# Performance work log

Hardware: AMD Instinct MI355X
Metric: run time of the kernel (lower is better)

## Reference

```python
import jax, jax.numpy as jnp
import numpy as np
import math

B, L, D = 8, 1024, 512
H, DK, DV = 8, 64, 64
DFC = 2048
EPS = 1e-5


def layernorm(x, g, b):
    mu = jnp.mean(x, axis=-1, keepdims=True)
    var = jnp.var(x, axis=-1, keepdims=True)
    return (x - mu) * jax.lax.rsqrt(var + EPS) * g + b


def setup_inputs() -> dict:
    key = jax.random.key(0)
    ks = jax.random.split(key, 12)
    s = 0.02
    return {
        "x": jax.random.normal(ks[0], (B, L, D), jnp.float32),
        "Wq": jax.random.normal(ks[1], (H * DK, D), jnp.float32) * s,
        "bq": jnp.zeros((H * DK,), jnp.float32),
        "Wk": jax.random.normal(ks[2], (H * DK, D), jnp.float32) * s,
        "bk": jnp.zeros((H * DK,), jnp.float32),
        "Wv": jax.random.normal(ks[3], (H * DV, D), jnp.float32) * s,
        "bv": jnp.zeros((H * DV,), jnp.float32),
        "Wo": jax.random.normal(ks[4], (D, H * DV), jnp.float32) * s,
        "bo": jnp.zeros((D,), jnp.float32),
        "conv1_w": jax.random.normal(ks[5], (DFC, D), jnp.float32) * s,
        "conv1_b": jnp.zeros((DFC,), jnp.float32),
        "ln1_g": jnp.ones((D,), jnp.float32),
        "ln1_b": jnp.zeros((D,), jnp.float32),
        "conv2_w": jax.random.normal(ks[6], (D, DFC), jnp.float32) * s,
        "conv2_b": jnp.zeros((D,), jnp.float32),
        "ln2_g": jnp.ones((D,), jnp.float32),
        "ln2_b": jnp.zeros((D,), jnp.float32),
    }


def reference(x, Wq, bq, Wk, bk, Wv, bv, Wo, bo, conv1_w, conv1_b,
              ln1_g, ln1_b, conv2_w, conv2_b, ln2_g, ln2_b):
    # Multihead attention (self-attn: x supplies Q,K and V)
    norm_fact = 1.0 / math.sqrt(D)
    Q = (x @ Wq.T + bq).reshape(B, L, H, DK)
    K = (x @ Wk.T + bk).reshape(B, L, H, DK)
    V = (x @ Wv.T + bv).reshape(B, L, H, DV)
    scores = jnp.einsum('blhe,bshe->bhls', Q, K) * norm_fact  # [B,H,L,L]
    scores = jax.nn.softmax(scores, axis=-1)
    attn_out = jnp.einsum('bhls,bshd->blhd', scores, V).reshape(B, L, H * DV)
    x_ = attn_out @ Wo.T + bo
    # residual + LayerNorm (dropout is identity in eval)
    x1 = layernorm(x + x_, ln1_g, ln1_b)
    # pointwise conv FFN (kernel_size=1 == linear over channels)
    y = jax.nn.relu(jnp.einsum('bld,fd->blf', x1, conv1_w) + conv1_b)
    y = jnp.einsum('blf,df->bld', y, conv2_w) + conv2_b
    return layernorm(x1 + y, ln2_g, ln2_b)
```

## Files before the change

### kernel.cpp

```cpp
#include <hip/hip_runtime.h>
#include <hip/hip_bf16.h>
#include <math.h>

#define Bp 8
#define Lp 1024
#define Dp 512
#define Hp 8
#define DFCp 2048
#define ROWS (Bp*Lp)
#define EPSp 1e-5f
#define SCALEp 0.04419417382415922f

typedef __bf16 bf16_t;
typedef __attribute__((ext_vector_type(8))) __bf16 bf16x8;
typedef __attribute__((ext_vector_type(4))) __bf16 bf16x4;
typedef __attribute__((ext_vector_type(4))) float f32x4;

__global__ __launch_bounds__(256) void f2b_all(
    const float* __restrict__ x,  const float* __restrict__ Wq,
    const float* __restrict__ Wk, const float* __restrict__ Wv,
    const float* __restrict__ Wo, const float* __restrict__ c1,
    const float* __restrict__ c2,
    bf16_t* __restrict__ xb, bf16_t* __restrict__ WQKVb,
    bf16_t* __restrict__ Wob, bf16_t* __restrict__ c1b,
    bf16_t* __restrict__ c2b)
{
    int i = blockIdx.x * 256 + threadIdx.x;
    const float* src; bf16_t* dst; int off;
    if      (i < 1048576) { src = x;  dst = xb;              off = i; }
    else if (i < 1114112) { src = Wq; dst = WQKVb;           off = i - 1048576; }
    else if (i < 1179648) { src = Wk; dst = WQKVb + 262144;  off = i - 1114112; }
    else if (i < 1245184) { src = Wv; dst = WQKVb + 524288;  off = i - 1179648; }
    else if (i < 1310720) { src = Wo; dst = Wob;             off = i - 1245184; }
    else if (i < 1572864) { src = c1; dst = c1b;             off = i - 1310720; }
    else                  { src = c2; dst = c2b;             off = i - 1572864; }
    float4 v = ((const float4*)src)[off];
    bf16x4 o;
    o[0] = (bf16_t)v.x; o[1] = (bf16_t)v.y; o[2] = (bf16_t)v.z; o[3] = (bf16_t)v.w;
    ((bf16x4*)dst)[off] = o;
}

__global__ __launch_bounds__(256) void pack_bias(const float* __restrict__ bq,
                                                 const float* __restrict__ bk,
                                                 const float* __restrict__ bv,
                                                 float* __restrict__ out) {
    int i = blockIdx.x * 256 + threadIdx.x;
    float v;
    if (i < 512) v = bq[i];
    else if (i < 1024) v = bk[i - 512];
    else v = bv[i - 1024];
    out[i] = v;
}

__device__ __forceinline__ void gload16(const bf16_t* g, bf16_t* l) {
    __builtin_amdgcn_global_load_lds(
        (const __attribute__((address_space(1))) void*)g,
        (__attribute__((address_space(3))) void*)l,
        16, 0, 0);
}

template<int OUT_BF16, int RELU, int SPLIT_V, int NT, int KSPLIT>
__global__ __launch_bounds__(256) void gemm_mfma(
    const bf16_t* __restrict__ A, const bf16_t* __restrict__ W,
    const float* __restrict__ bias, void* __restrict__ Cv,
    bf16_t* __restrict__ Ct, bf16_t* __restrict__ P0, bf16_t* __restrict__ P1,
    int M, int N, int Kd)
{
    constexpr int NJ = NT / 32;
    __shared__ bf16_t As[128 * 32];
    __shared__ bf16_t Bs[NT * 32];
    const int tid  = threadIdx.x;
    const int wave = tid >> 6;
    const int lane = tid & 63;
    const int row0 = blockIdx.y * 128;
    const int col0 = blockIdx.x * NT;
    const int wm = (wave >> 1) * 64;
    const int wn = (wave & 1) * (NT / 2);

    const int sr = lane >> 2;
    const int sc = (lane & 3) * 8;
    const int half = lane >> 4;
    const int mrow = lane & 15;

    f32x4 acc[4][NJ] = {};

    const bf16_t* Ag = A + (size_t)row0 * Kd;
    const bf16_t* Bg = W + (size_t)col0 * Kd;

    const int Kc = Kd / KSPLIT;
    const int kbeg = (KSPLIT > 1) ? blockIdx.z * Kc : 0;

    for (int k0 = kbeg; k0 < kbeg + Kc; k0 += 32) {
        __syncthreads();
        #pragma unroll
        for (int c = 0; c < 2; ++c) {
            const int chunk = c * 4 + wave;
            const int r = chunk * 16 + sr;
            gload16(Ag + (size_t)r * Kd + k0 + sc, &As[chunk * 512]);
        }
        #pragma unroll
        for (int c = 0; c < NT / 64; ++c) {
            const int chunk = c * 4 + wave;
            const int r = chunk * 16 + sr;
            gload16(Bg + (size_t)r * Kd + k0 + sc, &Bs[chunk * 512]);
        }
        __syncthreads();

        bf16x8 af[4], bfr[NJ];
        #pragma unroll
        for (int i = 0; i < 4; ++i)
            af[i] = *(const bf16x8*)&As[(wm + i * 16 + mrow) * 32 + half * 8];
        #pragma unroll
        for (int j = 0; j < NJ; ++j)
            bfr[j] = *(const bf16x8*)&Bs[(wn + j * 16 + mrow) * 32 + half * 8];
        #pragma unroll
        for (int i = 0; i < 4; ++i)
            #pragma unroll
            for (int j = 0; j < NJ; ++j)
                acc[i][j] = __builtin_amdgcn_mfma_f32_16x16x32_bf16(
                    af[i], bfr[j], acc[i][j], 0, 0, 0);
    }

    float* Cf = (float*)Cv;
    bf16_t* Cb = (bf16_t*)Cv;
    bf16_t* Pz = nullptr;
    if (KSPLIT > 1) {
        const int z = blockIdx.z;
        Pz = (z < 2 ? P0 : P1) + (size_t)(z & 1) * ((size_t)M * N);
    }
    #pragma unroll
    for (int i = 0; i < 4; ++i) {
        const int r = row0 + wm + i * 16 + (lane >> 4) * 4;
        #pragma unroll
        for (int j = 0; j < NJ; ++j) {
            const int c = col0 + wn + j * 16 + (lane & 15);
            if (KSPLIT > 1) {
                #pragma unroll
                for (int reg = 0; reg < 4; ++reg)
                    Pz[(size_t)(r + reg) * N + c] = (bf16_t)acc[i][j][reg];
            } else if (SPLIT_V && c >= 1024) {
                const float bv = bias[c];
                const int h = (c - 1024) >> 6, d = (c - 1024) & 63;
                const int b = r >> 10, l = r & 1023;
                bf16x4 v4;
                #pragma unroll
                for (int reg = 0; reg < 4; ++reg)
                    v4[reg] = (bf16_t)(acc[i][j][reg] + bv);
                *(bf16x4*)&Ct[(((size_t)b * 8 + h) * 64 + d) * 1024 + l] = v4;
            } else {
                const float bv = bias[c];
                #pragma unroll
                for (int reg = 0; reg < 4; ++reg) {
                    float v = acc[i][j][reg] + bv;
                    if (RELU) v = fmaxf(v, 0.0f);
                    if (OUT_BF16) Cb[(size_t)(r + reg) * N + c] = (bf16_t)v;
                    else          Cf[(size_t)(r + reg) * N + c] = v;
                }
            }
        }
    }
}

__global__ __launch_bounds__(256) void flash_attn_mfma(
    const bf16_t* __restrict__ QKV, const bf16_t* __restrict__ Vtg,
    bf16_t* __restrict__ out)
{
    const int qt = blockIdx.x;
    const int bh = blockIdx.y;
    const int b  = bh >> 3;
    const int h  = bh & 7;
    const int tid  = threadIdx.x;
    const int wave = tid >> 6;
    const int lane = tid & 63;
    const int li = lane & 15;
    const int lg = lane >> 4;

    __shared__ bf16_t Qs[64][72];
    __shared__ bf16_t Ks[64][72];
    __shared__ bf16_t Vt[64][72];
    __shared__ bf16_t Ps[64][72];

    const size_t qrow0  = (size_t)(b * Lp + qt * 64) * 1536 + h * 64;
    const size_t krow0  = (size_t)(b * Lp) * 1536 + 512 + h * 64;
    const size_t vtbase = (size_t)bh * 64 * 1024;

    const int sr = tid >> 3;
    const int sc = (tid & 7) * 8;

    #pragma unroll
    for (int i = 0; i < 2; ++i) {
        int row = i * 32 + sr;
        *(bf16x8*)&Qs[row][sc] = *(const bf16x8*)&QKV[qrow0 + (size_t)row * 1536 + sc];
    }
    __syncthreads();

    bf16x8 qa0 = *(const bf16x8*)&Qs[wave * 16 + li][lg * 8];
    bf16x8 qa1 = *(const bf16x8*)&Qs[wave * 16 + li][32 + lg * 8];

    f32x4 O[4] = {};
    float l_lane = 0.0f;

    for (int s0 = 0; s0 < Lp; s0 += 64) {
        __syncthreads();
        #pragma unroll
        for (int i = 0; i < 2; ++i) {
            int row = i * 32 + sr;
            *(bf16x8*)&Ks[row][sc] =
                *(const bf16x8*)&QKV[krow0 + (size_t)(s0 + row) * 1536 + sc];
            *(bf16x8*)&Vt[row][sc] =
                *(const bf16x8*)&Vtg[vtbase + (size_t)row * 1024 + s0 + sc];
        }
        __syncthreads();

        #pragma unroll
        for (int st = 0; st < 4; ++st) {
            bf16x8 kf0 = *(const bf16x8*)&Ks[st * 16 + li][lg * 8];
            bf16x8 kf1 = *(const bf16x8*)&Ks[st * 16 + li][32 + lg * 8];
            f32x4 z = {0.0f, 0.0f, 0.0f, 0.0f};
            z = __builtin_amdgcn_mfma_f32_16x16x32_bf16(kf0, qa0, z, 0, 0, 0);
            z = __builtin_amdgcn_mfma_f32_16x16x32_bf16(kf1, qa1, z, 0, 0, 0);
            bf16x4 p4;
            #pragma unroll
            for (int reg = 0; reg < 4; ++reg) {
                float p = __expf(z[reg] * SCALEp);
                l_lane += p;
                p4[reg] = (bf16_t)p;
            }
            *(bf16x4*)&Ps[wave * 16 + li][st * 16 + lg * 4] = p4;
        }

        bf16x8 pa0 = *(const bf16x8*)&Ps[wave * 16 + li][lg * 8];
        bf16x8 pa1 = *(const bf16x8*)&Ps[wave * 16 + li][32 + lg * 8];
        #pragma unroll
        for (int dt = 0; dt < 4; ++dt) {
            bf16x8 vf0 = *(const bf16x8*)&Vt[dt * 16 + li][lg * 8];
            bf16x8 vf1 = *(const bf16x8*)&Vt[dt * 16 + li][32 + lg * 8];
            O[dt] = __builtin_amdgcn_mfma_f32_16x16x32_bf16(pa0, vf0, O[dt], 0, 0, 0);
            O[dt] = __builtin_amdgcn_mfma_f32_16x16x32_bf16(pa1, vf1, O[dt], 0, 0, 0);
        }
    }

    float l_full = l_lane;
    l_full += __shfl_xor(l_full, 16);
    l_full += __shfl_xor(l_full, 32);

    #pragma unroll
    for (int reg = 0; reg < 4; ++reg) {
        const float lq = __shfl(l_full, lg * 4 + reg);
        const float inv = 1.0f / lq;
        const size_t row = (size_t)(b * Lp + qt * 64 + wave * 16 + lg * 4 + reg);
        #pragma unroll
        for (int dt = 0; dt < 4; ++dt) {
            out[row * Dp + h * 64 + dt * 16 + li] = (bf16_t)(O[dt][reg] * inv);
        }
    }
}

__global__ __launch_bounds__(256) void ln_residual(
    const float* __restrict__ a, const float* __restrict__ r,
    const float* __restrict__ g, const float* __restrict__ beta,
    float* __restrict__ out, bf16_t* __restrict__ outb)
{
    const int row = blockIdx.x;
    const int tid = threadIdx.x;
    const size_t base = (size_t)row * Dp;

    __shared__ float red1[256];
    __shared__ float red2[256];

    float v0 = a[base + tid] + r[base + tid];
    float v1 = a[base + tid + 256] + r[base + tid + 256];

    red1[tid] = v0 + v1;
    red2[tid] = v0 * v0 + v1 * v1;
    __syncthreads();
    for (int off = 128; off > 0; off >>= 1) {
        if (tid < off) {
            red1[tid] += red1[tid + off];
            red2[tid] += red2[tid + off];
        }
        __syncthreads();
    }
    const float mu  = red1[0] * (1.0f / Dp);
    const float var = red2[0] * (1.0f / Dp) - mu * mu;
    const float rstd = rsqrtf(var + EPSp);

    float o0 = (v0 - mu) * rstd * g[tid]       + beta[tid];
    float o1 = (v1 - mu) * rstd * g[tid + 256] + beta[tid + 256];
    out[base + tid]       = o0;
    out[base + tid + 256] = o1;
    outb[base + tid]       = (bf16_t)o0;
    outb[base + tid + 256] = (bf16_t)o1;
}

__global__ __launch_bounds__(256) void ln_residual_p4(
    const float* __restrict__ a,
    const bf16_t* __restrict__ P0, const bf16_t* __restrict__ P1,
    const float* __restrict__ bias,
    const float* __restrict__ g, const float* __restrict__ beta,
    float* __restrict__ out)
{
    const int row = blockIdx.x;
    const int tid = threadIdx.x;
    const size_t base = (size_t)row * Dp;
    const size_t MN = (size_t)ROWS * Dp;

    __shared__ float red1[256];
    __shared__ float red2[256];

    float y0 = (float)P0[base + tid] + (float)P0[MN + base + tid]
             + (float)P1[base + tid] + (float)P1[MN + base + tid] + bias[tid];
    float y1 = (float)P0[base + tid + 256] + (float)P0[MN + base + tid + 256]
             + (float)P1[base + tid + 256] + (float)P1[MN + base + tid + 256] + bias[tid + 256];
    float v0 = a[base + tid] + y0;
    float v1 = a[base + tid + 256] + y1;

    red1[tid] = v0 + v1;
    red2[tid] = v0 * v0 + v1 * v1;
    __syncthreads();
    for (int off = 128; off > 0; off >>= 1) {
        if (tid < off) {
            red1[tid] += red1[tid + off];
            red2[tid] += red2[tid + off];
        }
        __syncthreads();
    }
    const float mu  = red1[0] * (1.0f / Dp);
    const float var = red2[0] * (1.0f / Dp) - mu * mu;
    const float rstd = rsqrtf(var + EPSp);

    out[base + tid]       = (v0 - mu) * rstd * g[tid]       + beta[tid];
    out[base + tid + 256] = (v1 - mu) * rstd * g[tid + 256] + beta[tid + 256];
}

extern "C" void kernel_launch(void* const* d_in, const int* in_sizes, int n_in,
                              void* d_out, int out_size, void* d_ws, size_t ws_size,
                              hipStream_t stream)
{
    const float* x       = (const float*)d_in[0];
    const float* Wq      = (const float*)d_in[1];
    const float* bq      = (const float*)d_in[2];
    const float* Wk      = (const float*)d_in[3];
    const float* bk      = (const float*)d_in[4];
    const float* Wv      = (const float*)d_in[5];
    const float* bv      = (const float*)d_in[6];
    const float* Wo      = (const float*)d_in[7];
    const float* bo      = (const float*)d_in[8];
    const float* conv1_w = (const float*)d_in[9];
    const float* conv1_b = (const float*)d_in[10];
    const float* ln1_g   = (const float*)d_in[11];
    const float* ln1_b   = (const float*)d_in[12];
    const float* conv2_w = (const float*)d_in[13];
    const float* conv2_b = (const float*)d_in[14];
    const float* ln2_g   = (const float*)d_in[15];
    const float* ln2_b   = (const float*)d_in[16];

    char* w = (char*)d_ws;
    bf16_t* QKVb = (bf16_t*)w;
    bf16_t* Ab   = (bf16_t*)(w + 25165824);
    bf16_t* Hb   = (bf16_t*)w;
    char* w1     = w + 33554432;
    float* Xp    = (float*)w1;
    bf16_t* Part0 = (bf16_t*)w1;
    float* X1    = (float*)(w1 + 16777216);
    bf16_t* X1b  = (bf16_t*)(w1 + 2*16777216);
    bf16_t* Part1 = (bf16_t*)(w1 + 2*16777216 + 8388608);
    char* w2     = w1 + 3*16777216 + 8388608;
    bf16_t* xb     = (bf16_t*)w2;
    bf16_t* WQKVb  = (bf16_t*)(w2 + 8388608);
    bf16_t* Wob    = (bf16_t*)(w2 + 8388608 + 1572864);
    bf16_t* c1b    = (bf16_t*)(w2 + 8388608 + 1572864 + 524288);
    bf16_t* c2b    = (bf16_t*)(w2 + 8388608 + 1572864 + 524288 + 2097152);
    float*  bqkv   = (float*)(w2 + 8388608 + 1572864 + 524288 + 2*2097152);
    bf16_t* Vtg    = (bf16_t*)(w2 + 8388608 + 1572864 + 524288 + 2*2097152 + 8192);

    float* outp = (float*)d_out;
    dim3 blk(256);

    hipLaunchKernelGGL(f2b_all, dim3(7168), blk, 0, stream,
                       x, Wq, Wk, Wv, Wo, conv1_w, conv2_w,
                       xb, WQKVb, Wob, c1b, c2b);
    hipLaunchKernelGGL(pack_bias, dim3(6), blk, 0, stream, bq, bk, bv, bqkv);

    hipLaunchKernelGGL((gemm_mfma<1,0,1,128,1>), dim3(1536/128, ROWS/128), blk, 0, stream,
                       xb, WQKVb, bqkv, (void*)QKVb, Vtg, (bf16_t*)nullptr, (bf16_t*)nullptr,
                       ROWS, 1536, Dp);

    hipLaunchKernelGGL(flash_attn_mfma, dim3(Lp/64, Bp*Hp), blk, 0, stream, QKVb, Vtg, Ab);

    hipLaunchKernelGGL((gemm_mfma<0,0,0,64,1>), dim3(Dp/64, ROWS/128), blk, 0, stream,
                       Ab, Wob, bo, (void*)Xp, (bf16_t*)nullptr, (bf16_t*)nullptr, (bf16_t*)nullptr,
                       ROWS, Dp, Dp);

    hipLaunchKernelGGL(ln_residual, dim3(ROWS), blk, 0, stream,
                       x, Xp, ln1_g, ln1_b, X1, X1b);

    hipLaunchKernelGGL((gemm_mfma<1,1,0,128,1>), dim3(DFCp/128, ROWS/128), blk, 0, stream,
                       X1b, c1b, conv1_b, (void*)Hb, (bf16_t*)nullptr, (bf16_t*)nullptr, (bf16_t*)nullptr,
                       ROWS, DFCp, Dp);

    hipLaunchKernelGGL((gemm_mfma<1,0,0,128,4>), dim3(Dp/128, ROWS/128, 4), blk, 0, stream,
                       Hb, c2b, conv2_b, (void*)nullptr, (bf16_t*)nullptr, Part0, Part1,
                       ROWS, Dp, DFCp);

    hipLaunchKernelGGL(ln_residual_p4, dim3(ROWS), blk, 0, stream,
                       X1, Part0, Part1, conv2_b, ln2_g, ln2_b, outp);
}
```

Before: 269.2 us.

## Widen GEMM K-tile with swizzled LDS, wave-per-row LayerNorms, bf16 intermediates

The GEMM K-step doubles to 64, and an XOR swizzle on LDS columns is meant to avoid bank conflicts while halving the number of barriers per K. Both LayerNorm kernels now give each row to one wave, using vectorized loads and shuffle reductions in place of shared-memory tree reductions. The out-projection output and the X1 residual become bf16 rather than fp32, and conv2 uses split-K 2 with a 64-wide N tile. The bias packing is folded into the conversion kernel to save a launch. These changes cut memory traffic and synchronization, but storing residuals in bf16 costs some precision.

```diff
diff --git a/kernel.cpp b/kernel.cpp
--- a/kernel.cpp
+++ b/kernel.cpp
@@ -21,11 +21,23 @@
     const float* __restrict__ Wk, const float* __restrict__ Wv,
     const float* __restrict__ Wo, const float* __restrict__ c1,
     const float* __restrict__ c2,
+    const float* __restrict__ bq, const float* __restrict__ bk,
+    const float* __restrict__ bv,
     bf16_t* __restrict__ xb, bf16_t* __restrict__ WQKVb,
     bf16_t* __restrict__ Wob, bf16_t* __restrict__ c1b,
-    bf16_t* __restrict__ c2b)
+    bf16_t* __restrict__ c2b, float* __restrict__ bqkv)
 {
     int i = blockIdx.x * 256 + threadIdx.x;
+    if (i >= 1835392) return;
+    if (i >= 1835008) {
+        int j = i - 1835008;
+        const float* s; int off;
+        if (j < 128)      { s = bq; off = j; }
+        else if (j < 256) { s = bk; off = j - 128; }
+        else              { s = bv; off = j - 256; }
+        ((float4*)bqkv)[j] = ((const float4*)s)[off];
+        return;
+    }
     const float* src; bf16_t* dst; int off;
     if      (i < 1048576) { src = x;  dst = xb;              off = i; }
     else if (i < 1114112) { src = Wq; dst = WQKVb;           off = i - 1048576; }
@@ -40,18 +52,6 @@
     ((bf16x4*)dst)[off] = o;
 }
 
-__global__ __launch_bounds__(256) void pack_bias(const float* __restrict__ bq,
-                                                 const float* __restrict__ bk,
-                                                 const float* __restrict__ bv,
-                                                 float* __restrict__ out) {
-    int i = blockIdx.x * 256 + threadIdx.x;
-    float v;
-    if (i < 512) v = bq[i];
-    else if (i < 1024) v = bk[i - 512];
-    else v = bv[i - 1024];
-    out[i] = v;
-}
-
 __device__ __forceinline__ void gload16(const bf16_t* g, bf16_t* l) {
     __builtin_amdgcn_global_load_lds(
         (const __attribute__((address_space(1))) void*)g,
@@ -63,12 +63,12 @@
 __global__ __launch_bounds__(256) void gemm_mfma(
     const bf16_t* __restrict__ A, const bf16_t* __restrict__ W,
     const float* __restrict__ bias, void* __restrict__ Cv,
-    bf16_t* __restrict__ Ct, bf16_t* __restrict__ P0, bf16_t* __restrict__ P1,
+    bf16_t* __restrict__ Ct, bf16_t* __restrict__ P0,
     int M, int N, int Kd)
 {
     constexpr int NJ = NT / 32;
-    __shared__ bf16_t As[128 * 32];
-    __shared__ bf16_t Bs[NT * 32];
+    __shared__ bf16_t As[128 * 64];
+    __shared__ bf16_t Bs[NT * 64];
     const int tid  = threadIdx.x;
     const int wave = tid >> 6;
     const int lane = tid & 63;
@@ -77,9 +77,10 @@
     const int wm = (wave >> 1) * 64;
     const int wn = (wave & 1) * (NT / 2);
 
-    const int sr = lane >> 2;
-    const int sc = (lane & 3) * 8;
-    const int half = lane >> 4;
+    const int lrow   = lane >> 3;
+    const int lchunk = lane & 7;
+    const int scol   = ((lchunk ^ lrow) * 8);
+    const int lg   = lane >> 4;
     const int mrow = lane & 15;
 
     f32x4 acc[4][NJ] = {};
@@ -90,44 +91,49 @@
     const int Kc = Kd / KSPLIT;
     const int kbeg = (KSPLIT > 1) ? blockIdx.z * Kc : 0;
 
-    for (int k0 = kbeg; k0 < kbeg + Kc; k0 += 32) {
+    for (int k0 = kbeg; k0 < kbeg + Kc; k0 += 64) {
         __syncthreads();
         #pragma unroll
-        for (int c = 0; c < 2; ++c) {
-            const int chunk = c * 4 + wave;
-            const int r = chunk * 16 + sr;
-            gload16(Ag + (size_t)r * Kd + k0 + sc, &As[chunk * 512]);
-        }
-        #pragma unroll
-        for (int c = 0; c < NT / 64; ++c) {
-            const int chunk = c * 4 + wave;
-            const int r = chunk * 16 + sr;
-            gload16(Bg + (size_t)r * Kd + k0 + sc, &Bs[chunk * 512]);
+        for (int c = 0; c < 4; ++c) {
+            const int ch = c * 4 + wave;
+            const int r = ch * 8 + lrow;
+            gload16(Ag + (size_t)r * Kd + k0 + scol, &As[ch * 512]);
+        }
+        #pragma unroll
+        for (int c = 0; c < NT / 32; ++c) {
+            const int ch = c * 4 + wave;
+            const int r = ch * 8 + lrow;
+            gload16(Bg + (size_t)r * Kd + k0 + scol, &Bs[ch * 512]);
         }
         __syncthreads();
 
-        bf16x8 af[4], bfr[NJ];
-        #pragma unroll
-        for (int i = 0; i < 4; ++i)
-            af[i] = *(const bf16x8*)&As[(wm + i * 16 + mrow) * 32 + half * 8];
-        #pragma unroll
-        for (int j = 0; j < NJ; ++j)
-            bfr[j] = *(const bf16x8*)&Bs[(wn + j * 16 + mrow) * 32 + half * 8];
-        #pragma unroll
-        for (int i = 0; i < 4; ++i)
+        #pragma unroll
+        for (int kk = 0; kk < 2; ++kk) {
+            bf16x8 af[4], bfr[NJ];
+            const int lc = kk * 4 + lg;
             #pragma unroll
-            for (int j = 0; j < NJ; ++j)
-                acc[i][j] = __builtin_amdgcn_mfma_f32_16x16x32_bf16(
-                    af[i], bfr[j], acc[i][j], 0, 0, 0);
+            for (int i = 0; i < 4; ++i) {
+                const int r = wm + i * 16 + mrow;
+                af[i] = *(const bf16x8*)&As[r * 64 + ((lc ^ (r & 7)) * 8)];
+            }
+            #pragma unroll
+            for (int j = 0; j < NJ; ++j) {
+                const int r = wn + j * 16 + mrow;
+                bfr[j] = *(const bf16x8*)&Bs[r * 64 + ((lc ^ (r & 7)) * 8)];
+            }
+            #pragma unroll
+            for (int i = 0; i < 4; ++i)
+                #pragma unroll
+                for (int j = 0; j < NJ; ++j)
+                    acc[i][j] = __builtin_amdgcn_mfma_f32_16x16x32_bf16(
+                        af[i], bfr[j], acc[i][j], 0, 0, 0);
+        }
     }
 
     float* Cf = (float*)Cv;
     bf16_t* Cb = (bf16_t*)Cv;
     bf16_t* Pz = nullptr;
-    if (KSPLIT > 1) {
-        const int z = blockIdx.z;
-        Pz = (z < 2 ? P0 : P1) + (size_t)(z & 1) * ((size_t)M * N);
-    }
+    if (KSPLIT > 1) Pz = P0 + (size_t)blockIdx.z * ((size_t)M * N);
     #pragma unroll
     for (int i = 0; i < 4; ++i) {
         const int r = row0 + wm + i * 16 + (lane >> 4) * 4;
@@ -256,81 +262,96 @@
     }
 }
 
-__global__ __launch_bounds__(256) void ln_residual(
-    const float* __restrict__ a, const float* __restrict__ r,
+__global__ __launch_bounds__(256) void ln1_fused(
+    const float* __restrict__ x, const bf16_t* __restrict__ xpb,
     const float* __restrict__ g, const float* __restrict__ beta,
-    float* __restrict__ out, bf16_t* __restrict__ outb)
-{
-    const int row = blockIdx.x;
-    const int tid = threadIdx.x;
-    const size_t base = (size_t)row * Dp;
-
-    __shared__ float red1[256];
-    __shared__ float red2[256];
-
-    float v0 = a[base + tid] + r[base + tid];
-    float v1 = a[base + tid + 256] + r[base + tid + 256];
-
-    red1[tid] = v0 + v1;
-    red2[tid] = v0 * v0 + v1 * v1;
-    __syncthreads();
-    for (int off = 128; off > 0; off >>= 1) {
-        if (tid < off) {
-            red1[tid] += red1[tid + off];
-            red2[tid] += red2[tid + off];
-        }
-        __syncthreads();
-    }
-    const float mu  = red1[0] * (1.0f / Dp);
-    const float var = red2[0] * (1.0f / Dp) - mu * mu;
-    const float rstd = rsqrtf(var + EPSp);
-
-    float o0 = (v0 - mu) * rstd * g[tid]       + beta[tid];
-    float o1 = (v1 - mu) * rstd * g[tid + 256] + beta[tid + 256];
-    out[base + tid]       = o0;
-    out[base + tid + 256] = o1;
-    outb[base + tid]       = (bf16_t)o0;
-    outb[base + tid + 256] = (bf16_t)o1;
-}
-
-__global__ __launch_bounds__(256) void ln_residual_p4(
-    const float* __restrict__ a,
-    const bf16_t* __restrict__ P0, const bf16_t* __restrict__ P1,
+    bf16_t* __restrict__ x1b)
+{
+    const int wave = threadIdx.x >> 6;
+    const int lane = threadIdx.x & 63;
+    const int row  = blockIdx.x * 4 + wave;
+    const int col  = lane * 8;
+    const size_t base = (size_t)row * Dp + col;
+
+    float4 a0 = *(const float4*)&x[base];
+    float4 a1 = *(const float4*)&x[base + 4];
+    bf16x8 p  = *(const bf16x8*)&xpb[base];
+    float v[8] = { a0.x + (float)p[0], a0.y + (float)p[1],
+                   a0.z + (float)p[2], a0.w + (float)p[3],
+                   a1.x + (float)p[4], a1.y + (float)p[5],
+                   a1.z + (float)p[6], a1.w + (float)p[7] };
+    float s = 0.0f, q = 0.0f;
+    #pragma unroll
+    for (int t = 0; t < 8; ++t) { s += v[t]; q += v[t] * v[t]; }
+    #pragma unroll
+    for (int off = 1; off < 64; off <<= 1) {
+        s += __shfl_xor(s, off);
+        q += __shfl_xor(q, off);
+    }
+    const float mu = s * (1.0f / Dp);
+    const float rstd = rsqrtf(q * (1.0f / Dp) - mu * mu + EPSp);
+
+    float4 g0 = *(const float4*)&g[col],    g1 = *(const float4*)&g[col + 4];
+    float4 b0 = *(const float4*)&beta[col], b1 = *(const float4*)&beta[col + 4];
+    bf16x8 o;
+    o[0] = (bf16_t)((v[0] - mu) * rstd * g0.x + b0.x);
+    o[1] = (bf16_t)((v[1] - mu) * rstd * g0.y + b0.y);
+    o[2] = (bf16_t)((v[2] - mu) * rstd * g0.z + b0.z);
+    o[3] = (bf16_t)((v[3] - mu) * rstd * g0.w + b0.w);
+    o[4] = (bf16_t)((v[4] - mu) * rstd * g1.x + b1.x);
+    o[5] = (bf16_t)((v[5] - mu) * rstd * g1.y + b1.y);
+    o[6] = (bf16_t)((v[6] - mu) * rstd * g1.z + b1.z);
+    o[7] = (bf16_t)((v[7] - mu) * rstd * g1.w + b1.w);
+    *(bf16x8*)&x1b[base] = o;
+}
+
+__global__ __launch_bounds__(256) void ln2_fused(
+    const bf16_t* __restrict__ x1b, const bf16_t* __restrict__ P0,
     const float* __restrict__ bias,
     const float* __restrict__ g, const float* __restrict__ beta,
     float* __restrict__ out)
 {
-    const int row = blockIdx.x;
-    const int tid = threadIdx.x;
-    const size_t base = (size_t)row * Dp;
+    const int wave = threadIdx.x >> 6;
+    const int lane = threadIdx.x & 63;
+    const int row  = blockIdx.x * 4 + wave;
+    const int col  = lane * 8;
+    const size_t base = (size_t)row * Dp + col;
     const size_t MN = (size_t)ROWS * Dp;
 
-    __shared__ float red1[256];
-    __shared__ float red2[256];
-
-    float y0 = (float)P0[base + tid] + (float)P0[MN + base + tid]
-             + (float)P1[base + tid] + (float)P1[MN + base + tid] + bias[tid];
-    float y1 = (float)P0[base + tid + 256] + (float)P0[MN + base + tid + 256]
-             + (float)P1[base + tid + 256] + (float)P1[MN + base + tid + 256] + bias[tid + 256];
-    float v0 = a[base + tid] + y0;
-    float v1 = a[base + tid + 256] + y1;
-
-    red1[tid] = v0 + v1;
-    red2[tid] = v0 * v0 + v1 * v1;
-    __syncthreads();
-    for (int off = 128; off > 0; off >>= 1) {
-        if (tid < off) {
-            red1[tid] += red1[tid + off];
-            red2[tid] += red2[tid + off];
-        }
-        __syncthreads();
-    }
-    const float mu  = red1[0] * (1.0f / Dp);
-    const float var = red2[0] * (1.0f / Dp) - mu * mu;
-    const float rstd = rsqrtf(var + EPSp);
-
-    out[base + tid]       = (v0 - mu) * rstd * g[tid]       + beta[tid];
-    out[base + tid + 256] = (v1 - mu) * rstd * g[tid + 256] + beta[tid + 256];
+    bf16x8 x1 = *(const bf16x8*)&x1b[base];
+    bf16x8 pa = *(const bf16x8*)&P0[base];
+    bf16x8 pb = *(const bf16x8*)&P0[MN + base];
+    float4 c0 = *(const float4*)&bias[col], c1 = *(const float4*)&bias[col + 4];
+    const float cb[8] = { c0.x, c0.y, c0.z, c0.w, c1.x, c1.y, c1.z, c1.w };
+    float v[8];
+    #pragma unroll
+    for (int t = 0; t < 8; ++t)
+        v[t] = (float)x1[t] + (float)pa[t] + (float)pb[t] + cb[t];
+
+    float s = 0.0f, q = 0.0f;
+    #pragma unroll
+    for (int t = 0; t < 8; ++t) { s += v[t]; q += v[t] * v[t]; }
+    #pragma unroll
+    for (int off = 1; off < 64; off <<= 1) {
+        s += __shfl_xor(s, off);
+        q += __shfl_xor(q, off);
+    }
+    const float mu = s * (1.0f / Dp);
+    const float rstd = rsqrtf(q * (1.0f / Dp) - mu * mu + EPSp);
+
+    float4 g0 = *(const float4*)&g[col],    g1 = *(const float4*)&g[col + 4];
+    float4 b0 = *(const float4*)&beta[col], b1 = *(const float4*)&beta[col + 4];
+    float4 o0, o1;
+    o0.x = (v[0] - mu) * rstd * g0.x + b0.x;
+    o0.y = (v[1] - mu) * rstd * g0.y + b0.y;
+    o0.z = (v[2] - mu) * rstd * g0.z + b0.z;
+    o0.w = (v[3] - mu) * rstd * g0.w + b0.w;
+    o1.x = (v[4] - mu) * rstd * g1.x + b1.x;
+    o1.y = (v[5] - mu) * rstd * g1.y + b1.y;
+    o1.z = (v[6] - mu) * rstd * g1.z + b1.z;
+    o1.w = (v[7] - mu) * rstd * g1.w + b1.w;
+    *(float4*)&out[base]     = o0;
+    *(float4*)&out[base + 4] = o1;
 }
 
 extern "C" void kernel_launch(void* const* d_in, const int* in_sizes, int n_in,
@@ -360,12 +381,10 @@
     bf16_t* Ab   = (bf16_t*)(w + 25165824);
     bf16_t* Hb   = (bf16_t*)w;
     char* w1     = w + 33554432;
-    float* Xp    = (float*)w1;
+    bf16_t* Xpb  = (bf16_t*)w1;
     bf16_t* Part0 = (bf16_t*)w1;
-    float* X1    = (float*)(w1 + 16777216);
-    bf16_t* X1b  = (bf16_t*)(w1 + 2*16777216);
-    bf16_t* Part1 = (bf16_t*)(w1 + 2*16777216 + 8388608);
-    char* w2     = w1 + 3*16777216 + 8388608;
+    bf16_t* X1b  = (bf16_t*)(w1 + 16777216);
+    char* w2     = w1 + 25165824;
     bf16_t* xb     = (bf16_t*)w2;
     bf16_t* WQKVb  = (bf16_t*)(w2 + 8388608);
     bf16_t* Wob    = (bf16_t*)(w2 + 8388608 + 1572864);
@@ -377,32 +396,31 @@
     float* outp = (float*)d_out;
     dim3 blk(256);
 
-    hipLaunchKernelGGL(f2b_all, dim3(7168), blk, 0, stream,
-                       x, Wq, Wk, Wv, Wo, conv1_w, conv2_w,
-                       xb, WQKVb, Wob, c1b, c2b);
-    hipLaunchKernelGGL(pack_bias, dim3(6), blk, 0, stream, bq, bk, bv, bqkv);
+    hipLaunchKernelGGL(f2b_all, dim3(7170), blk, 0, stream,
+                       x, Wq, Wk, Wv, Wo, conv1_w, conv2_w, bq, bk, bv,
+                       xb, WQKVb, Wob, c1b, c2b, bqkv);
 
     hipLaunchKernelGGL((gemm_mfma<1,0,1,128,1>), dim3(1536/128, ROWS/128), blk, 0, stream,
-                       xb, WQKVb, bqkv, (void*)QKVb, Vtg, (bf16_t*)nullptr, (bf16_t*)nullptr,
+                       xb, WQKVb, bqkv, (void*)QKVb, Vtg, (bf16_t*)nullptr,
                        ROWS, 1536, Dp);
 
     hipLaunchKernelGGL(flash_attn_mfma, dim3(Lp/64, Bp*Hp), blk, 0, stream, QKVb, Vtg, Ab);
 
-    hipLaunchKernelGGL((gemm_mfma<0,0,0,64,1>), dim3(Dp/64, ROWS/128), blk, 0, stream,
-                       Ab, Wob, bo, (void*)Xp, (bf16_t*)nullptr, (bf16_t*)nullptr, (bf16_t*)nullptr,
+    hipLaunchKernelGGL((gemm_mfma<1,0,0,64,1>), dim3(Dp/64, ROWS/128), blk, 0, stream,
+                       Ab, Wob, bo, (void*)Xpb, (bf16_t*)nullptr, (bf16_t*)nullptr,
                        ROWS, Dp, Dp);
 
-    hipLaunchKernelGGL(ln_residual, dim3(ROWS), blk, 0, stream,
-                       x, Xp, ln1_g, ln1_b, X1, X1b);
+    hipLaunchKernelGGL(ln1_fused, dim3(ROWS/4), blk, 0, stream,
+                       x, Xpb, ln1_g, ln1_b, X1b);
 
     hipLaunchKernelGGL((gemm_mfma<1,1,0,128,1>), dim3(DFCp/128, ROWS/128), blk, 0, stream,
-                       X1b, c1b, conv1_b, (void*)Hb, (bf16_t*)nullptr, (bf16_t*)nullptr, (bf16_t*)nullptr,
+                       X1b, c1b, conv1_b, (void*)Hb, (bf16_t*)nullptr, (bf16_t*)nullptr,
                        ROWS, DFCp, Dp);
 
-    hipLaunchKernelGGL((gemm_mfma<1,0,0,128,4>), dim3(Dp/128, ROWS/128, 4), blk, 0, stream,
-                       Hb, c2b, conv2_b, (void*)nullptr, (bf16_t*)nullptr, Part0, Part1,
+    hipLaunchKernelGGL((gemm_mfma<1,0,0,64,2>), dim3(Dp/64, ROWS/128, 2), blk, 0, stream,
+                       Hb, c2b, conv2_b, (void*)nullptr, (bf16_t*)nullptr, Part0,
                        ROWS, Dp, DFCp);
 
-    hipLaunchKernelGGL(ln_residual_p4, dim3(ROWS), blk, 0, stream,
-                       X1, Part0, Part1, conv2_b, ln2_g, ln2_b, outp);
-}
+    hipLaunchKernelGGL(ln2_fused, dim3(ROWS/4), blk, 0, stream,
+                       X1b, Part0, conv2_b, ln2_g, ln2_b, outp);
+}
```

Result: faster. 260.7 us (-3.1%).
